# Optimization experiments

Hardware: AMD Instinct MI355X
Metric: run time of the kernel (lower is better)

The kernel has to match this reference:

```python
import jax, jax.numpy as jnp
import numpy as np

# ---- config (from DAREConfig init_kwargs) ----
TAU = 0.1
RHO_VIS = 0.5          # is_visual=True -> rho_target = rho_vis_target
PREFIX_KAPPA = 64
LAMBDA_RATIO = 1.0
LAMBDA_SOFT = 0.1
LAMBDA_HARD = 1.0

B, S = 256, 32768


def setup_inputs() -> dict:
    key = jax.random.key(0)
    k1, k2 = jax.random.split(key)
    importance = jax.random.normal(k1, (B, S), dtype=jnp.float32)
    modality_mask = jax.random.randint(k2, (B, S), 0, 2) > 0  # bool [B,S]
    return {"importance": importance, "modality_mask": modality_mask}


def reference(importance, modality_mask):
    """Vectorized DAREController.route(is_visual=True, training=True).

    The torch loop over batch with data-dependent k is replaced by a
    per-row k-th-largest threshold: for each row, k_b = min(int(rho*|mm_b|),
    |valid_b|); tokens with score >= k_b-th largest valid score are kept
    (this matches DifferentiableTopK's hard mask soft>0.5, i.e. exactly the
    top-k scores, assuming no ties).
    """
    mm = modality_mask.astype(bool)          # [B,S]
    b, s = importance.shape

    target = jnp.clip(mm.sum(axis=1).astype(jnp.float32) * RHO_VIS, 1.0)  # [B]
    prefix = jnp.arange(s) < min(PREFIX_KAPPA, s)                          # [S]
    eff = mm & ~prefix[None, :]                                            # [B,S] routable tokens
    n_valid = eff.sum(axis=1)                                              # [B]
    k = jnp.minimum(target.astype(jnp.int32), n_valid)                     # [B] per-row top-k size

    neg_inf = jnp.float32(-jnp.inf)
    masked = jnp.where(eff, importance, neg_inf)                           # [B,S]
    sorted_desc = -jnp.sort(-masked, axis=1)                               # [B,S]
    idx = jnp.clip(k - 1, 0, s - 1)                                        # [B]
    thresh = jnp.take_along_axis(sorted_desc, idx[:, None], axis=1)        # [B,1]
    hard = masked >= thresh                                                # top-k of valid tokens

    keep_mask = prefix[None, :] | (hard & (k > 0)[:, None])                # [B,S]

    # ---- training / is_visual losses ----
    kept = (keep_mask & mm).sum(axis=1).astype(jnp.float32)
    denom = mm.sum(axis=1).astype(jnp.float32) + 1e-6
    actual_ratio = kept / denom
    loss_ratio = jnp.mean(jnp.abs(actual_ratio - RHO_VIS))                 # F.l1_loss

    dropped = mm & ~keep_mask
    n_drop = dropped.sum()
    drop_mean = jnp.sum(jnp.where(dropped, importance, 0.0)) / jnp.maximum(n_drop, 1).astype(jnp.float32)
    loss_soft = jnp.where(n_drop > 0, drop_mean, 0.0)

    loss_hard = jnp.mean(jnp.clip(RHO_VIS - actual_ratio, 0.0))

    return (keep_mask,
            LAMBDA_RATIO * loss_ratio,
            LAMBDA_SOFT * loss_soft,
            LAMBDA_HARD * loss_hard)
```

## Files before the change

kernel.cpp:

```cpp
#include <hip/hip_runtime.h>


#define NB 256
#define NS 32768
#define KAPPA 64
#define NT 1024
#define V4 (NS / NT / 4)

__device__ __forceinline__ unsigned int fkey(float f) {
    unsigned int u = __float_as_uint(f);
    return (u & 0x80000000u) ? ~u : (u | 0x80000000u);
}

__device__ __forceinline__ float unkey(unsigned int k) {
    unsigned int u = (k & 0x80000000u) ? (k ^ 0x80000000u) : ~k;
    return __uint_as_float(u);
}

__global__ __launch_bounds__(NT) void dare_rows(const float* __restrict__ imp,
                                                const int* __restrict__ mask,
                                                float* __restrict__ keep,
                                                float* __restrict__ stats) {
    __shared__ unsigned int hist[256];
    __shared__ unsigned int wtot[4];
    __shared__ unsigned int sh_mm, sh_eff;
    __shared__ unsigned int sh_pref;
    __shared__ unsigned int sh_rem;
    __shared__ unsigned int sh_kept, sh_ndrop;
    __shared__ float sh_dsum;

    const int row = blockIdx.x;
    const int tid = threadIdx.x;
    const int lane = tid & 63;
    const float4* rimp4  = (const float4*)(imp  + (size_t)row * NS);
    const int4*   rmask4 = (const int4*)  (mask + (size_t)row * NS);
    float4*       rkeep4 = (float4*)      (keep + (size_t)row * NS);

    if (tid < 256) hist[tid] = 0;
    if (tid == 0) {
        sh_mm = 0; sh_eff = 0; sh_kept = 0; sh_ndrop = 0; sh_dsum = 0.0f;
        sh_pref = 0; sh_rem = 1;
    }
    __syncthreads();

    unsigned int keys[V4 * 4];
    unsigned int effbits = 0, mmbits = 0;

    #pragma unroll
    for (int i = 0; i < V4; i++) {
        const int idx4 = tid + i * NT;
        const float4 v = rimp4[idx4];
        const int4   m = rmask4[idx4];
        const float vv[4] = {v.x, v.y, v.z, v.w};
        const int    mv[4] = {m.x, m.y, m.z, m.w};
        #pragma unroll
        for (int j = 0; j < 4; j++) {
            const int e = i * 4 + j;
            const int col = idx4 * 4 + j;
            keys[e] = fkey(vv[j]);
            const bool mm  = (mv[j] != 0);
            const bool eff = mm && (col >= KAPPA);
            mmbits  |= (mm  ? 1u : 0u) << e;
            effbits |= (eff ? 1u : 0u) << e;
            if (eff) atomicAdd(&hist[keys[e] >> 24], 1u);
        }
    }

    int mm_local  = __popc(mmbits);
    int eff_local = __popc(effbits);
    #pragma unroll
    for (int off = 32; off; off >>= 1) {
        mm_local  += __shfl_down(mm_local, off);
        eff_local += __shfl_down(eff_local, off);
    }
    if (lane == 0) {
        atomicAdd(&sh_mm,  (unsigned int)mm_local);
        atomicAdd(&sh_eff, (unsigned int)eff_local);
    }
    __syncthreads();

    #pragma unroll
    for (int pass = 0; pass < 4; pass++) {
        const int shift = 24 - 8 * pass;

        if (pass > 0) {
            if (tid < 256) hist[tid] = 0;
            __syncthreads();
            const unsigned int pmask = 0xFFFFFFFFu << (shift + 8);
            const unsigned int pref = sh_pref;
            #pragma unroll
            for (int e = 0; e < V4 * 4; e++) {
                const bool match = ((effbits >> e) & 1u) && ((keys[e] & pmask) == pref);
                if (match) atomicAdd(&hist[(keys[e] >> shift) & 0xFFu], 1u);
            }
            __syncthreads();
        }

        unsigned int h = 0, s = 0;
        if (tid < 256) {
            h = hist[tid];
            s = h;
            #pragma unroll
            for (int off = 1; off < 64; off <<= 1) {
                const unsigned int t = __shfl_down(s, off);
                if (lane + off < 64) s += t;
            }
            if (lane == 0) wtot[tid >> 6] = s;
        }
        __syncthreads();
        if (tid < 256) {
            unsigned int sfull = s;
            for (int w = (tid >> 6) + 1; w < 4; w++) sfull += wtot[w];
            unsigned int rem;
            if (pass == 0) {
                const float target = fmaxf((float)sh_mm * 0.5f, 1.0f);
                const int k = min((int)target, (int)sh_eff);
                rem = (unsigned int)max(k, 1);
            } else {
                rem = sh_rem;
            }
            if (sfull >= rem && (sfull - h) < rem) {
                sh_pref = (pass == 0) ? ((unsigned int)tid << 24)
                                      : (sh_pref | ((unsigned int)tid << shift));
                sh_rem = rem - (sfull - h);
            }
        }
        __syncthreads();
    }

    const unsigned int thresh = sh_pref;
    const float targetf = fmaxf((float)sh_mm * 0.5f, 1.0f);
    const bool kpos = (min((int)targetf, (int)sh_eff) > 0);

    int kept_l = 0, ndrop_l = 0;
    float dsum_l = 0.0f;
    #pragma unroll
    for (int i = 0; i < V4; i++) {
        const int idx4 = tid + i * NT;
        float ov[4];
        #pragma unroll
        for (int j = 0; j < 4; j++) {
            const int e = i * 4 + j;
            const int col = idx4 * 4 + j;
            const bool mm  = (mmbits >> e) & 1u;
            const bool eff = (effbits >> e) & 1u;
            const bool hard = eff && kpos && (keys[e] >= thresh);
            const bool kp = (col < KAPPA) || hard;
            ov[j] = kp ? 1.0f : 0.0f;
            kept_l += (kp && mm) ? 1 : 0;
            const bool drop = mm && !kp;
            ndrop_l += drop ? 1 : 0;
            dsum_l += drop ? unkey(keys[e]) : 0.0f;
        }
        float4 o; o.x = ov[0]; o.y = ov[1]; o.z = ov[2]; o.w = ov[3];
        rkeep4[idx4] = o;
    }
    #pragma unroll
    for (int off = 32; off; off >>= 1) {
        kept_l  += __shfl_down(kept_l, off);
        ndrop_l += __shfl_down(ndrop_l, off);
        dsum_l  += __shfl_down(dsum_l, off);
    }
    if (lane == 0) {
        atomicAdd(&sh_kept,  (unsigned int)kept_l);
        atomicAdd(&sh_ndrop, (unsigned int)ndrop_l);
        atomicAdd(&sh_dsum,  dsum_l);
    }
    __syncthreads();
    if (tid == 0) {
        stats[row * 4 + 0] = (float)sh_kept;
        stats[row * 4 + 1] = (float)sh_mm;
        stats[row * 4 + 2] = (float)sh_ndrop;
        stats[row * 4 + 3] = sh_dsum;
    }
}

__global__ __launch_bounds__(256) void dare_losses(const float* __restrict__ stats,
                                                   float* __restrict__ out) {
    __shared__ float w_a[4], w_h[4], w_n[4], w_d[4];
    const int tid = threadIdx.x;
    const float kept = stats[tid * 4 + 0];
    const float mmc  = stats[tid * 4 + 1];
    const float nd   = stats[tid * 4 + 2];
    const float ds   = stats[tid * 4 + 3];
    const float ratio = kept / (mmc + 1e-6f);
    float a = fabsf(ratio - 0.5f);
    float h = fmaxf(0.5f - ratio, 0.0f);
    float n = nd, d = ds;
    #pragma unroll
    for (int off = 32; off; off >>= 1) {
        a += __shfl_down(a, off);
        h += __shfl_down(h, off);
        n += __shfl_down(n, off);
        d += __shfl_down(d, off);
    }
    const int wid = tid >> 6, lane = tid & 63;
    if (lane == 0) { w_a[wid] = a; w_h[wid] = h; w_n[wid] = n; w_d[wid] = d; }
    __syncthreads();
    if (tid == 0) {
        float sa = 0.f, shh = 0.f, sn = 0.f, sd = 0.f;
        for (int w = 0; w < 4; w++) { sa += w_a[w]; shh += w_h[w]; sn += w_n[w]; sd += w_d[w]; }
        out[0] = sa / (float)NB;
        out[1] = (sn > 0.0f) ? 0.1f * (sd / fmaxf(sn, 1.0f)) : 0.0f;
        out[2] = shh / (float)NB;
    }
}

extern "C" void kernel_launch(void* const* d_in, const int* in_sizes, int n_in,
                              void* d_out, int out_size, void* d_ws, size_t ws_size,
                              hipStream_t stream) {
    const float* imp  = (const float*)d_in[0];
    const int*   mask = (const int*)d_in[1];
    float* out   = (float*)d_out;
    float* stats = (float*)d_ws;

    dare_rows<<<NB, NT, 0, stream>>>(imp, mask, out, stats);
    dare_losses<<<1, 256, 0, stream>>>(stats, out + (size_t)NB * NS);
}
```

Baseline: 111.4 us.

## Use per-wave privatized first-pass histograms and nontemporal loads/stores

After: 117.5 us. +5.4%, slower.

```diff
diff --git a/kernel.cpp b/kernel.cpp
--- a/kernel.cpp
+++ b/kernel.cpp
@@ -5,7 +5,12 @@
 #define NS 32768
 #define KAPPA 64
 #define NT 1024
+#define NW (NT / 64)
+#define HP 257
 #define V4 (NS / NT / 4)
+
+typedef float f32x4 __attribute__((ext_vector_type(4)));
+typedef int   i32x4 __attribute__((ext_vector_type(4)));
 
 __device__ __forceinline__ unsigned int fkey(float f) {
     unsigned int u = __float_as_uint(f);
@@ -21,6 +26,7 @@
                                                 const int* __restrict__ mask,
                                                 float* __restrict__ keep,
                                                 float* __restrict__ stats) {
+    __shared__ unsigned int hist0[NW * HP];
     __shared__ unsigned int hist[256];
     __shared__ unsigned int wtot[4];
     __shared__ unsigned int sh_mm, sh_eff;
@@ -32,10 +38,12 @@
     const int row = blockIdx.x;
     const int tid = threadIdx.x;
     const int lane = tid & 63;
-    const float4* rimp4  = (const float4*)(imp  + (size_t)row * NS);
-    const int4*   rmask4 = (const int4*)  (mask + (size_t)row * NS);
-    float4*       rkeep4 = (float4*)      (keep + (size_t)row * NS);
-
+    const int wid = tid >> 6;
+    const f32x4* rimp4  = (const f32x4*)(imp  + (size_t)row * NS);
+    const i32x4* rmask4 = (const i32x4*)(mask + (size_t)row * NS);
+    f32x4*       rkeep4 = (f32x4*)      (keep + (size_t)row * NS);
+
+    for (int i = tid; i < NW * HP; i += NT) hist0[i] = 0;
     if (tid < 256) hist[tid] = 0;
     if (tid == 0) {
         sh_mm = 0; sh_eff = 0; sh_kept = 0; sh_ndrop = 0; sh_dsum = 0.0f;
@@ -45,24 +53,23 @@
 
     unsigned int keys[V4 * 4];
     unsigned int effbits = 0, mmbits = 0;
+    unsigned int* myhist = &hist0[wid * HP];
 
     #pragma unroll
     for (int i = 0; i < V4; i++) {
         const int idx4 = tid + i * NT;
-        const float4 v = rimp4[idx4];
-        const int4   m = rmask4[idx4];
-        const float vv[4] = {v.x, v.y, v.z, v.w};
-        const int    mv[4] = {m.x, m.y, m.z, m.w};
+        const f32x4 v = __builtin_nontemporal_load(&rimp4[idx4]);
+        const i32x4 m = __builtin_nontemporal_load(&rmask4[idx4]);
         #pragma unroll
         for (int j = 0; j < 4; j++) {
             const int e = i * 4 + j;
             const int col = idx4 * 4 + j;
-            keys[e] = fkey(vv[j]);
-            const bool mm  = (mv[j] != 0);
+            keys[e] = fkey(v[j]);
+            const bool mm  = (m[j] != 0);
             const bool eff = mm && (col >= KAPPA);
             mmbits  |= (mm  ? 1u : 0u) << e;
             effbits |= (eff ? 1u : 0u) << e;
-            if (eff) atomicAdd(&hist[keys[e] >> 24], 1u);
+            if (eff) atomicAdd(&myhist[keys[e] >> 24], 1u);
         }
     }
 
@@ -98,7 +105,12 @@
 
         unsigned int h = 0, s = 0;
         if (tid < 256) {
-            h = hist[tid];
+            if (pass == 0) {
+                #pragma unroll
+                for (int w = 0; w < NW; w++) h += hist0[w * HP + tid];
+            } else {
+                h = hist[tid];
+            }
             s = h;
             #pragma unroll
             for (int off = 1; off < 64; off <<= 1) {
@@ -137,7 +149,7 @@
     #pragma unroll
     for (int i = 0; i < V4; i++) {
         const int idx4 = tid + i * NT;
-        float ov[4];
+        f32x4 o;
         #pragma unroll
         for (int j = 0; j < 4; j++) {
             const int e = i * 4 + j;
@@ -146,14 +158,13 @@
             const bool eff = (effbits >> e) & 1u;
             const bool hard = eff && kpos && (keys[e] >= thresh);
             const bool kp = (col < KAPPA) || hard;
-            ov[j] = kp ? 1.0f : 0.0f;
+            o[j] = kp ? 1.0f : 0.0f;
             kept_l += (kp && mm) ? 1 : 0;
             const bool drop = mm && !kp;
             ndrop_l += drop ? 1 : 0;
             dsum_l += drop ? unkey(keys[e]) : 0.0f;
         }
-        float4 o; o.x = ov[0]; o.y = ov[1]; o.z = ov[2]; o.w = ov[3];
-        rkeep4[idx4] = o;
+        __builtin_nontemporal_store(o, &rkeep4[idx4]);
     }
     #pragma unroll
     for (int off = 32; off; off >>= 1) {
```
